# Optimization experiments

Hardware: AMD Instinct MI355X
Metric: run time of the kernel (lower is better)

The kernel has to match this reference:

```python
import jax, jax.numpy as jnp
import numpy as np

PS = 8        # window/patch size (win_size)
STRIDE = 4    # overlapping-window stride
HEADS = 2


def _rel_pos_index(ps):
    ch = np.arange(ps)
    coords = np.stack(np.meshgrid(ch, ch, indexing='ij'))  # (2, ps, ps)
    cf = coords.reshape(2, -1)
    rel = cf[:, :, None] - cf[:, None, :]                   # (2, L, L)
    rel = rel.transpose(1, 2, 0).copy()
    rel[:, :, 0] += ps - 1
    rel[:, :, 1] += ps - 1
    rel[:, :, 0] *= 2 * ps - 1
    return rel.sum(-1).astype(np.int32)                     # (L, L)


def setup_inputs() -> dict:
    key = jax.random.key(0)
    ks = jax.random.split(key, 6)
    t, h, w, c = 8, 128, 128, 32
    inp = {
        'x': jax.random.normal(ks[0], (t, h, w, c), jnp.float32),
        'qkv_w': jax.random.normal(ks[1], (3 * c, c), jnp.float32) * (c ** -0.5),
        'qkv_b': jnp.zeros((3 * c,), jnp.float32),
        'rel_pos_table': jax.random.normal(ks[2], ((2 * PS - 1) ** 2, HEADS), jnp.float32) * 0.02,
        'proj_w': jax.random.normal(ks[3], (c, c), jnp.float32) * (c ** -0.5),
        'proj_b': jnp.zeros((c,), jnp.float32),
        'rel_pos_index': jnp.asarray(_rel_pos_index(PS)),
    }
    return inp


def reference(x, qkv_w, qkv_b, rel_pos_table, proj_w, proj_b, rel_pos_index):
    t, h, w, c = x.shape
    hd = c // HEADS
    scale = hd ** -0.5
    L = PS * PS
    nh = (h - 1) // STRIDE + 1
    nw = (w - 1) // STRIDE + 1

    # --- iUnfold: gather overlapping ps x ps patches with reflected borders ---
    r0 = jnp.arange(nh) * STRIDE
    c0 = jnp.arange(nw) * STRIDE
    ridx = r0[:, None] + jnp.arange(PS)[None, :]            # (nh, ps)
    cidx = c0[:, None] + jnp.arange(PS)[None, :]            # (nw, ps)
    ridx = jnp.where(ridx >= h, 2 * (h - 1) - ridx, ridx)
    cidx = jnp.where(cidx >= w, 2 * (w - 1) - cidx, cidx)
    # advanced indexing -> (t, nh, nw, ps, ps, c)
    patches = x[:, ridx[:, None, :, None], cidx[None, :, None, :], :]
    n = t * nh * nw
    patches = patches.reshape(n, L, c)

    # --- LinearProjection qkv ---
    qkv = patches @ qkv_w.T + qkv_b                          # (n, L, 3c)
    q, k, v = jnp.split(qkv, 3, axis=-1)
    def heads(a):
        return a.reshape(n, L, HEADS, hd).transpose(0, 2, 1, 3)  # (n, H, L, hd)
    q, k, v = heads(q), heads(k), heads(v)

    # --- scaled attention + indexed relative position bias ---
    attn = jnp.einsum('nhld,nhmd->nhlm', q * scale, k)       # (n, H, L, L)
    bias = rel_pos_table[rel_pos_index]                      # (L, L, H)
    attn = jax.nn.softmax(attn + bias.transpose(2, 0, 1)[None], axis=-1)
    out = jnp.einsum('nhlm,nhmd->nhld', attn, v)             # (n, H, L, hd)
    out = out.transpose(0, 2, 1, 3).reshape(n, L, c)
    out = out @ proj_w.T + proj_b

    # --- iFold: scatter-add with overlap-count (wfold) normalization ---
    lin = (ridx[:, None, :, None] * w + cidx[None, :, None, :]).reshape(-1)  # (nh*nw*L,)
    vals = out.reshape(t, nh * nw * L, c)
    vid = jnp.zeros((t, h * w, c), x.dtype).at[:, lin, :].add(vals)
    cnt = jnp.zeros((h * w,), x.dtype).at[lin].add(1.0)
    vid = vid / (cnt[None, :, None] + 1e-10)
    return vid.reshape(t, h, w, c)
```

## Files before the change

### kernel.cpp

```cpp
#include <hip/hip_runtime.h>
#include <hip/hip_bf16.h>
#include <stdint.h>

typedef __attribute__((ext_vector_type(8))) short bf16x8;
typedef __attribute__((ext_vector_type(4))) float f32x4;

#define LOG2E 1.44269504088896340736f
#define QSCALE (0.25f * LOG2E)

#define WS_BIASF 0u
#define WS_QKVW  32768u
#define WS_PROJW 38912u
#define WS_QKVB  40960u
#define WS_OUT   41472u
#define NEED_FULL (41472ull + 8192ull*64*32*2)

#define PWAVE 4096

__device__ __forceinline__ uint32_t pk2(float a, float b){
    union{__hip_bfloat162 h;uint32_t u;}c;
    c.h=__float22bfloat162_rn(make_float2(a,b)); return c.u;
}
template<int OFF>
__device__ __forceinline__ uint2 tr16(uint32_t a){
    uint2 d;
    asm volatile("ds_read_b64_tr_b16 %0, %1 offset:%2" : "=v"(d) : "v"(a), "i"(OFF) : "memory");
    return d;
}
__device__ __forceinline__ void lgkm0(){
    asm volatile("s_waitcnt lgkmcnt(0)" ::: "memory");
    __builtin_amdgcn_sched_barrier(0);
}
__device__ __forceinline__ bf16x8 mk8u(uint2 a, uint2 b){
    union{bf16x8 v;uint32_t u[4];}z; z.u[0]=a.x; z.u[1]=a.y; z.u[2]=b.x; z.u[3]=b.y; return z.v;
}
__device__ __forceinline__ bf16x8 mk8q(uint32_t q0, uint32_t q1, uint32_t q2, uint32_t q3){
    union{bf16x8 v;uint32_t u[4];}z; z.u[0]=q0; z.u[1]=q1; z.u[2]=q2; z.u[3]=q3; return z.v;
}
__device__ __forceinline__ void pl32(uint32_t &a, uint32_t &b){
    asm volatile("v_permlane32_swap_b32 %0, %1" : "+v"(a), "+v"(b));
}
__device__ __forceinline__ void pl16(uint32_t &a, uint32_t &b){
    asm volatile("v_permlane16_swap_b32 %0, %1" : "+v"(a), "+v"(b));
}
__device__ __forceinline__ f32x4 mfma16(uint2 a, uint2 b, f32x4 c){
    asm("v_mfma_f32_16x16x16_bf16 %0, %1, %2, %0" : "+v"(c) : "v"(a), "v"(b));
    return c;
}

__global__ __launch_bounds__(256) void prep(const float* __restrict__ qkv_w,
                                            const float* __restrict__ qkv_b,
                                            const float* __restrict__ rel_tab,
                                            const float* __restrict__ proj_w,
                                            char* __restrict__ ws)
{
    int t = blockIdx.x*256 + threadIdx.x;
    if (t < 2048) {
        int lanei = t & 63, tile = t >> 6;
        int h = tile >> 4, nt = (tile >> 2) & 3, mt = tile & 3;
        int gg = lanei >> 4, lnn = lanei & 15;
        int l = 16*nt + lnn;
        f32x4 v;
        #pragma unroll
        for (int r = 0; r < 4; ++r) {
            int m = 16*mt + 4*gg + r;
            int dr = (l >> 3) - (m >> 3) + 7;
            int dc = (l & 7) - (m & 7) + 7;
            v[r] = rel_tab[(dr*15 + dc)*2 + h] * LOG2E;
        }
        *(f32x4*)(ws + WS_BIASF + (size_t)t*16) = v;
    } else if (t < 3584) {
        int e = (t - 2048) * 2;
        int row = e >> 5;
        float s = (row < 32) ? QSCALE : 1.0f;
        *(uint32_t*)(ws + WS_QKVW + e*2) = pk2(qkv_w[e]*s, qkv_w[e+1]*s);
    } else {
        int e = (t - 3584) * 2;
        *(uint32_t*)(ws + WS_PROJW + e*2) = pk2(proj_w[e], proj_w[e+1]);
    }
    if (t < 96) {
        float s = (t < 32) ? QSCALE : 1.0f;
        ((float*)(ws + WS_QKVB))[t] = qkv_b[t] * s;
    }
}

template<int WSPATH>
__global__ __launch_bounds__(128, 4) void win_attn(
    const float* __restrict__ x, const float* __restrict__ proj_b,
    const char* __restrict__ wsc, uint16_t* __restrict__ wout,
    float* __restrict__ out)
{
    __shared__ __align__(16) char smem_all[2*PWAVE];
    const int tid = threadIdx.x;
    const int wv = tid >> 6, lane = tid & 63;
    const int g = lane >> 4, ln = lane & 15;
    const int bid = blockIdx.x;
    const int sb = (bid & 7) * 512 + (bid >> 3);
    const int wid = sb * 2 + wv;
    const int t_i = wid >> 10, wi = (wid >> 5) & 31, wj = wid & 31;
    char* smem = smem_all + wv * PWAVE;
    const uint32_t Lb = (uint32_t)(uintptr_t)(&smem[0]);

    const f32x4* biasF = (const f32x4*)(wsc + WS_BIASF);
    const uint16_t* wbf = (const uint16_t*)(wsc + WS_QKVW);
    const float* qbs = (const float*)(wsc + WS_QKVB);

    int pixb[4];
    #pragma unroll
    for (int i = 0; i < 4; ++i) {
        int tok = 16*i + ln, pr = tok >> 3, pc = tok & 7;
        int ar = wi*4 + pr; if (ar >= 128) ar = 254 - ar;
        int ac = wj*4 + pc; if (ac >= 128) ac = 254 - ac;
        pixb[i] = (t_i*128 + ar)*128 + ac;
    }

    bf16x8 xf[4];
    #pragma unroll
    for (int nt = 0; nt < 4; ++nt) {
        const float4* p = (const float4*)(x + (size_t)pixb[nt]*32 + 8*g);
        float4 a = p[0], b = p[1];
        union{bf16x8 v; uint32_t u[4];} z;
        z.u[0]=pk2(a.x,a.y); z.u[1]=pk2(a.z,a.w);
        z.u[2]=pk2(b.x,b.y); z.u[3]=pk2(b.z,b.w);
        xf[nt] = z.v;
    }

    uint2 qk[4][4];
    #pragma unroll
    for (int mt = 0; mt < 6; ++mt) {
        bf16x8 wf = *(const bf16x8*)(wbf + (ln + 16*mt)*32 + 8*g);
        float4 qb = *(const float4*)(qbs + 16*mt + 4*g);
        #pragma unroll
        for (int nt = 0; nt < 4; ++nt) {
            f32x4 acc = {qb.x, qb.y, qb.z, qb.w};
            acc = __builtin_amdgcn_mfma_f32_16x16x32_bf16(wf, xf[nt], acc, 0, 0, 0);
            if (mt < 4) {
                qk[mt][nt].x = pk2(acc[0], acc[1]);
                qk[mt][nt].y = pk2(acc[2], acc[3]);
            } else {
                int tok = 16*nt + ln;
                uint2 u; u.x = pk2(acc[0], acc[1]); u.y = pk2(acc[2], acc[3]);
                *(uint2*)(smem + (mt-4)*2048 + tok*32 + 8*g) = u;
            }
        }
    }

    const uint32_t one2 = 0x3f803f80u;
    const bf16x8 ones = mk8q(one2, one2, one2, one2);

    #pragma unroll
    for (int h = 0; h < 2; ++h) {
        uint32_t va = Lb + h*2048 + 256*g + 8*ln;
        uint2 v00 = tr16<0>(va),    v01 = tr16<128>(va);
        uint2 v10 = tr16<1024>(va), v11 = tr16<1152>(va);
        lgkm0();
        bf16x8 vb0 = mk8u(v00, v01), vb1 = mk8u(v10, v11);

        f32x4 bpc[4];
        #pragma unroll
        for (int mt = 0; mt < 4; ++mt)
            bpc[mt] = biasF[((h*4 + 0)*4 + mt)*64 + lane];

        #pragma unroll
        for (int nt = 0; nt < 4; ++nt) {
            f32x4 bpn[4];
            const int ntn = (nt < 3) ? nt + 1 : 3;
            #pragma unroll
            for (int mt = 0; mt < 4; ++mt)
                bpn[mt] = biasF[((h*4 + ntn)*4 + mt)*64 + lane];

            __builtin_amdgcn_s_setprio(1);
            f32x4 sc[4];
            #pragma unroll
            for (int mt = 0; mt < 4; ++mt)
                sc[mt] = mfma16(qk[2+h][mt], qk[h][nt], bpc[mt]);
            __builtin_amdgcn_s_setprio(0);

            #pragma unroll
            for (int mt = 0; mt < 4; ++mt) {
                sc[mt][0]=__builtin_amdgcn_exp2f(sc[mt][0]);
                sc[mt][1]=__builtin_amdgcn_exp2f(sc[mt][1]);
                sc[mt][2]=__builtin_amdgcn_exp2f(sc[mt][2]);
                sc[mt][3]=__builtin_amdgcn_exp2f(sc[mt][3]);
            }

            uint32_t pkA[4], pkB[4];
            #pragma unroll
            for (int mt = 0; mt < 4; ++mt) {
                pkA[mt] = pk2(sc[mt][0], sc[mt][1]);
                pkB[mt] = pk2(sc[mt][2], sc[mt][3]);
            }
            uint32_t a0 = pkA[0], a1 = pkA[1]; pl32(a0, a1); pl16(a0, a1);
            uint32_t b0 = pkB[0], b1 = pkB[1]; pl32(b0, b1); pl16(b0, b1);
            bf16x8 pa0 = mk8q(a0, b0, a1, b1);
            uint32_t a2 = pkA[2], a3 = pkA[3]; pl32(a2, a3); pl16(a2, a3);
            uint32_t b2 = pkB[2], b3 = pkB[3]; pl32(b2, b3); pl16(b2, b3);
            bf16x8 pa1 = mk8q(a2, b2, a3, b3);

            __builtin_amdgcn_s_setprio(1);
            f32x4 z = {0.f,0.f,0.f,0.f};
            z = __builtin_amdgcn_mfma_f32_16x16x32_bf16(pa0, vb0, z, 0, 0, 0);
            f32x4 oc = __builtin_amdgcn_mfma_f32_16x16x32_bf16(pa1, vb1, z, 0, 0, 0);
            f32x4 sm = {0.f,0.f,0.f,0.f};
            sm = __builtin_amdgcn_mfma_f32_16x16x32_bf16(pa0, ones, sm, 0, 0, 0);
            sm = __builtin_amdgcn_mfma_f32_16x16x32_bf16(pa1, ones, sm, 0, 0, 0);
            __builtin_amdgcn_s_setprio(0);

            oc[0] *= __builtin_amdgcn_rcpf(sm[0]);
            oc[1] *= __builtin_amdgcn_rcpf(sm[1]);
            oc[2] *= __builtin_amdgcn_rcpf(sm[2]);
            oc[3] *= __builtin_amdgcn_rcpf(sm[3]);

            uint2 u; u.x = pk2(oc[0], oc[1]); u.y = pk2(oc[2], oc[3]);
            *(uint2*)(smem + h*2048 + (nt*4 + (ln>>2))*128 + (ln&3)*32 + 8*g) = u;

            #pragma unroll
            for (int mt = 0; mt < 4; ++mt) bpc[mt] = bpn[mt];
        }
    }

    const uint16_t* pwbf = (const uint16_t*)(wsc + WS_PROJW);
    bf16x8 w2f[2];
    w2f[0] = *(const bf16x8*)(pwbf + ln*32 + 8*g);
    w2f[1] = *(const bf16x8*)(pwbf + (16 + ln)*32 + 8*g);
    float4 pbv[2];
    pbv[0] = *(const float4*)(proj_b + 4*g);
    pbv[1] = *(const float4*)(proj_b + 16 + 4*g);

    uint32_t ob = Lb + ((uint32_t)(g >> 1) << 11) + ((uint32_t)(g & 1) << 8) + 8*ln;
    uint2 a0=tr16<0>(ob),    a1=tr16<128>(ob);
    uint2 b0=tr16<512>(ob),  b1=tr16<640>(ob);
    uint2 c0=tr16<1024>(ob), c1=tr16<1152>(ob);
    uint2 d0=tr16<1536>(ob), d1=tr16<1664>(ob);
    lgkm0();
    bf16x8 oa[4];
    oa[0]=mk8u(a0,a1); oa[1]=mk8u(b0,b1); oa[2]=mk8u(c0,c1); oa[3]=mk8u(d0,d1);

    #pragma unroll
    for (int mt2 = 0; mt2 < 2; ++mt2) {
        #pragma unroll
        for (int nt = 0; nt < 4; ++nt) {
            f32x4 acc = {pbv[mt2].x, pbv[mt2].y, pbv[mt2].z, pbv[mt2].w};
            acc = __builtin_amdgcn_mfma_f32_16x16x32_bf16(w2f[mt2], oa[nt], acc, 0, 0, 0);
            if (WSPATH) {
                uint2 u; u.x = pk2(acc[0], acc[1]); u.y = pk2(acc[2], acc[3]);
                *(uint2*)(wout + ((size_t)wid*64 + 16*nt + ln)*32 + 16*mt2 + 4*g) = u;
            } else {
                #pragma unroll
                for (int r = 0; r < 4; ++r)
                    atomicAdd(out + (size_t)pixb[nt]*32 + 16*mt2 + 4*g + r, acc[r]);
            }
        }
    }
}

__global__ __launch_bounds__(256) void gather_out(const uint16_t* __restrict__ ws,
                                                  float* __restrict__ out)
{
    int gid = blockIdx.x * 256 + threadIdx.x;
    int q = gid & 7;
    int c = (gid >> 3) & 127;
    int r = (gid >> 10) & 127;
    int t = gid >> 17;

    int wr[3], pr[3], nr = 0;
    { int w0 = r >> 2;
      wr[0] = w0; pr[0] = r & 3; nr = 1;
      if (w0 >= 1) { wr[nr] = w0 - 1; pr[nr] = (r & 3) + 4; nr++; }
      if (r >= 123 && r <= 126) { wr[nr] = 31; pr[nr] = 130 - r; nr++; } }
    int wc[3], pc[3], nc = 0;
    { int w0 = c >> 2;
      wc[0] = w0; pc[0] = c & 3; nc = 1;
      if (w0 >= 1) { wc[nc] = w0 - 1; pc[nc] = (c & 3) + 4; nc++; }
      if (c >= 123 && c <= 126) { wc[nc] = 31; pc[nc] = 130 - c; nc++; } }

    float4 acc; acc.x = acc.y = acc.z = acc.w = 0.f;
    #pragma unroll
    for (int i = 0; i < 3; ++i) {
        #pragma unroll
        for (int j = 0; j < 3; ++j) {
            if (i < nr && j < nc) {
                int win = t*1024 + wr[i]*32 + wc[j];
                int tok = pr[i]*8 + pc[j];
                ushort4 v = *reinterpret_cast<const ushort4*>(ws + ((size_t)win*64 + tok)*32 + q*4);
                union { uint32_t u; float f; } a0,a1,a2,a3;
                a0.u = (uint32_t)v.x << 16; a1.u = (uint32_t)v.y << 16;
                a2.u = (uint32_t)v.z << 16; a3.u = (uint32_t)v.w << 16;
                acc.x += a0.f; acc.y += a1.f; acc.z += a2.f; acc.w += a3.f;
            }
        }
    }
    float inv = __builtin_amdgcn_rcpf((float)(nr*nc));
    acc.x *= inv; acc.y *= inv; acc.z *= inv; acc.w *= inv;
    reinterpret_cast<float4*>(out)[gid] = acc;
}

__global__ __launch_bounds__(256) void div_kernel(float* __restrict__ out)
{
    int gid = blockIdx.x*blockDim.x + threadIdx.x;
    const int total4 = 8*128*128*32/4;
    if (gid >= total4) return;
    int pix = gid >> 3;
    int c_ = pix % 128;
    int r_ = (pix / 128) % 128;
    int cr = 0, cc = 0;
    for (int i = 0; i < 32; ++i) {
        #pragma unroll
        for (int p = 0; p < 8; ++p) {
            int rr = i*4 + p; if (rr >= 128) rr = 254 - rr;
            cr += (rr == r_);
            int aa = i*4 + p; if (aa >= 128) aa = 254 - aa;
            cc += (aa == c_);
        }
    }
    float inv = 1.f / ((float)cr*(float)cc + 1e-10f);
    float4* p4 = reinterpret_cast<float4*>(out) + gid;
    float4 v = *p4;
    v.x *= inv; v.y *= inv; v.z *= inv; v.w *= inv;
    *p4 = v;
}

extern "C" void kernel_launch(void* const* d_in, const int* in_sizes, int n_in,
                              void* d_out, int out_size, void* d_ws, size_t ws_size,
                              hipStream_t stream) {
    const float* x       = (const float*)d_in[0];
    const float* qkv_w   = (const float*)d_in[1];
    const float* qkv_b   = (const float*)d_in[2];
    const float* rel_tab = (const float*)d_in[3];
    const float* proj_w  = (const float*)d_in[4];
    const float* proj_b  = (const float*)d_in[5];
    float* out = (float*)d_out;
    char* ws = (char*)d_ws;

    prep<<<16, 256, 0, stream>>>(qkv_w, qkv_b, rel_tab, proj_w, ws);

    if (ws_size >= NEED_FULL) {
        win_attn<1><<<4096, 128, 0, stream>>>(x, proj_b, (const char*)ws,
                                              (uint16_t*)(ws + WS_OUT), out);
        gather_out<<<4096, 256, 0, stream>>>((const uint16_t*)(ws + WS_OUT), out);
    } else {
        hipMemsetAsync(out, 0, (size_t)out_size*sizeof(float), stream);
        win_attn<0><<<4096, 128, 0, stream>>>(x, proj_b, (const char*)ws, nullptr, out);
        const int tot4 = 8*128*128*32/4;
        div_kernel<<<(tot4 + 255)/256, 256, 0, stream>>>(out);
    }
}
```

Before: 50.31 us.

## Split attention heads across waves, one wave per head per window

The window-attention kernel now runs 256 threads per block, with two waves per window, each handling one attention head. Each wave computes only its head's Q, K and V projection, runs that head's attention, then after a block barrier computes half of the output projection channels. The intent is more wave-level parallelism and a shorter serial chain per wave, with fewer live registers per wave. The cost is that each pair of waves loads the same input pixels twice, plus a __syncthreads before the projection.

```diff
diff --git a/kernel.cpp b/kernel.cpp
--- a/kernel.cpp
+++ b/kernel.cpp
@@ -15,7 +15,7 @@
 #define WS_OUT   41472u
 #define NEED_FULL (41472ull + 8192ull*64*32*2)
 
-#define PWAVE 4096
+#define PWIN 4096
 
 __device__ __forceinline__ uint32_t pk2(float a, float b){
     union{__hip_bfloat162 h;uint32_t u;}c;
@@ -85,20 +85,21 @@
 }
 
 template<int WSPATH>
-__global__ __launch_bounds__(128, 4) void win_attn(
+__global__ __launch_bounds__(256, 6) void win_attn(
     const float* __restrict__ x, const float* __restrict__ proj_b,
     const char* __restrict__ wsc, uint16_t* __restrict__ wout,
     float* __restrict__ out)
 {
-    __shared__ __align__(16) char smem_all[2*PWAVE];
+    __shared__ __align__(16) char smem_all[2*PWIN];
     const int tid = threadIdx.x;
-    const int wv = tid >> 6, lane = tid & 63;
+    const int w = tid >> 6, lane = tid & 63;
+    const int wvwin = w & 1, h = w >> 1;
     const int g = lane >> 4, ln = lane & 15;
     const int bid = blockIdx.x;
     const int sb = (bid & 7) * 512 + (bid >> 3);
-    const int wid = sb * 2 + wv;
+    const int wid = sb * 2 + wvwin;
     const int t_i = wid >> 10, wi = (wid >> 5) & 31, wj = wid & 31;
-    char* smem = smem_all + wv * PWAVE;
+    char* smem = smem_all + wvwin * PWIN;
     const uint32_t Lb = (uint32_t)(uintptr_t)(&smem[0]);
 
     const f32x4* biasF = (const f32x4*)(wsc + WS_BIASF);
@@ -125,22 +126,26 @@
         xf[nt] = z.v;
     }
 
-    uint2 qk[4][4];
-    #pragma unroll
-    for (int mt = 0; mt < 6; ++mt) {
-        bf16x8 wf = *(const bf16x8*)(wbf + (ln + 16*mt)*32 + 8*g);
-        float4 qb = *(const float4*)(qbs + 16*mt + 4*g);
+    uint2 qkQ[4], qkK[4];
+    #pragma unroll
+    for (int j = 0; j < 3; ++j) {
+        const int mtw = 2*j + h;
+        bf16x8 wf = *(const bf16x8*)(wbf + (ln + 16*mtw)*32 + 8*g);
+        float4 qb = *(const float4*)(qbs + 16*mtw + 4*g);
         #pragma unroll
         for (int nt = 0; nt < 4; ++nt) {
             f32x4 acc = {qb.x, qb.y, qb.z, qb.w};
             acc = __builtin_amdgcn_mfma_f32_16x16x32_bf16(wf, xf[nt], acc, 0, 0, 0);
-            if (mt < 4) {
-                qk[mt][nt].x = pk2(acc[0], acc[1]);
-                qk[mt][nt].y = pk2(acc[2], acc[3]);
+            if (j == 0) {
+                qkQ[nt].x = pk2(acc[0], acc[1]);
+                qkQ[nt].y = pk2(acc[2], acc[3]);
+            } else if (j == 1) {
+                qkK[nt].x = pk2(acc[0], acc[1]);
+                qkK[nt].y = pk2(acc[2], acc[3]);
             } else {
                 int tok = 16*nt + ln;
                 uint2 u; u.x = pk2(acc[0], acc[1]); u.y = pk2(acc[2], acc[3]);
-                *(uint2*)(smem + (mt-4)*2048 + tok*32 + 8*g) = u;
+                *(uint2*)(smem + h*2048 + tok*32 + 8*g) = u;
             }
         }
     }
@@ -148,84 +153,79 @@
     const uint32_t one2 = 0x3f803f80u;
     const bf16x8 ones = mk8q(one2, one2, one2, one2);
 
-    #pragma unroll
-    for (int h = 0; h < 2; ++h) {
-        uint32_t va = Lb + h*2048 + 256*g + 8*ln;
-        uint2 v00 = tr16<0>(va),    v01 = tr16<128>(va);
-        uint2 v10 = tr16<1024>(va), v11 = tr16<1152>(va);
-        lgkm0();
-        bf16x8 vb0 = mk8u(v00, v01), vb1 = mk8u(v10, v11);
-
-        f32x4 bpc[4];
+    uint32_t va = Lb + h*2048 + 256*g + 8*ln;
+    uint2 v00 = tr16<0>(va),    v01 = tr16<128>(va);
+    uint2 v10 = tr16<1024>(va), v11 = tr16<1152>(va);
+    lgkm0();
+    bf16x8 vb0 = mk8u(v00, v01), vb1 = mk8u(v10, v11);
+
+    f32x4 bpc[4];
+    #pragma unroll
+    for (int mt = 0; mt < 4; ++mt)
+        bpc[mt] = biasF[((h*4 + 0)*4 + mt)*64 + lane];
+
+    #pragma unroll
+    for (int nt = 0; nt < 4; ++nt) {
+        f32x4 bpn[4];
+        const int ntn = (nt < 3) ? nt + 1 : 3;
         #pragma unroll
         for (int mt = 0; mt < 4; ++mt)
-            bpc[mt] = biasF[((h*4 + 0)*4 + mt)*64 + lane];
-
-        #pragma unroll
-        for (int nt = 0; nt < 4; ++nt) {
-            f32x4 bpn[4];
-            const int ntn = (nt < 3) ? nt + 1 : 3;
-            #pragma unroll
-            for (int mt = 0; mt < 4; ++mt)
-                bpn[mt] = biasF[((h*4 + ntn)*4 + mt)*64 + lane];
-
-            __builtin_amdgcn_s_setprio(1);
-            f32x4 sc[4];
-            #pragma unroll
-            for (int mt = 0; mt < 4; ++mt)
-                sc[mt] = mfma16(qk[2+h][mt], qk[h][nt], bpc[mt]);
-            __builtin_amdgcn_s_setprio(0);
-
-            #pragma unroll
-            for (int mt = 0; mt < 4; ++mt) {
-                sc[mt][0]=__builtin_amdgcn_exp2f(sc[mt][0]);
-                sc[mt][1]=__builtin_amdgcn_exp2f(sc[mt][1]);
-                sc[mt][2]=__builtin_amdgcn_exp2f(sc[mt][2]);
-                sc[mt][3]=__builtin_amdgcn_exp2f(sc[mt][3]);
-            }
-
-            uint32_t pkA[4], pkB[4];
-            #pragma unroll
-            for (int mt = 0; mt < 4; ++mt) {
-                pkA[mt] = pk2(sc[mt][0], sc[mt][1]);
-                pkB[mt] = pk2(sc[mt][2], sc[mt][3]);
-            }
-            uint32_t a0 = pkA[0], a1 = pkA[1]; pl32(a0, a1); pl16(a0, a1);
-            uint32_t b0 = pkB[0], b1 = pkB[1]; pl32(b0, b1); pl16(b0, b1);
-            bf16x8 pa0 = mk8q(a0, b0, a1, b1);
-            uint32_t a2 = pkA[2], a3 = pkA[3]; pl32(a2, a3); pl16(a2, a3);
-            uint32_t b2 = pkB[2], b3 = pkB[3]; pl32(b2, b3); pl16(b2, b3);
-            bf16x8 pa1 = mk8q(a2, b2, a3, b3);
-
-            __builtin_amdgcn_s_setprio(1);
-            f32x4 z = {0.f,0.f,0.f,0.f};
-            z = __builtin_amdgcn_mfma_f32_16x16x32_bf16(pa0, vb0, z, 0, 0, 0);
-            f32x4 oc = __builtin_amdgcn_mfma_f32_16x16x32_bf16(pa1, vb1, z, 0, 0, 0);
-            f32x4 sm = {0.f,0.f,0.f,0.f};
-            sm = __builtin_amdgcn_mfma_f32_16x16x32_bf16(pa0, ones, sm, 0, 0, 0);
-            sm = __builtin_amdgcn_mfma_f32_16x16x32_bf16(pa1, ones, sm, 0, 0, 0);
-            __builtin_amdgcn_s_setprio(0);
-
-            oc[0] *= __builtin_amdgcn_rcpf(sm[0]);
-            oc[1] *= __builtin_amdgcn_rcpf(sm[1]);
-            oc[2] *= __builtin_amdgcn_rcpf(sm[2]);
-            oc[3] *= __builtin_amdgcn_rcpf(sm[3]);
-
-            uint2 u; u.x = pk2(oc[0], oc[1]); u.y = pk2(oc[2], oc[3]);
-            *(uint2*)(smem + h*2048 + (nt*4 + (ln>>2))*128 + (ln&3)*32 + 8*g) = u;
-
-            #pragma unroll
-            for (int mt = 0; mt < 4; ++mt) bpc[mt] = bpn[mt];
-        }
-    }
+            bpn[mt] = biasF[((h*4 + ntn)*4 + mt)*64 + lane];
+
+        __builtin_amdgcn_s_setprio(1);
+        f32x4 sc[4];
+        #pragma unroll
+        for (int mt = 0; mt < 4; ++mt)
+            sc[mt] = mfma16(qkK[mt], qkQ[nt], bpc[mt]);
+        __builtin_amdgcn_s_setprio(0);
+
+        #pragma unroll
+        for (int mt = 0; mt < 4; ++mt) {
+            sc[mt][0]=__builtin_amdgcn_exp2f(sc[mt][0]);
+            sc[mt][1]=__builtin_amdgcn_exp2f(sc[mt][1]);
+            sc[mt][2]=__builtin_amdgcn_exp2f(sc[mt][2]);
+            sc[mt][3]=__builtin_amdgcn_exp2f(sc[mt][3]);
+        }
+
+        uint32_t pkA[4], pkB[4];
+        #pragma unroll
+        for (int mt = 0; mt < 4; ++mt) {
+            pkA[mt] = pk2(sc[mt][0], sc[mt][1]);
+            pkB[mt] = pk2(sc[mt][2], sc[mt][3]);
+        }
+        uint32_t a0 = pkA[0], a1 = pkA[1]; pl32(a0, a1); pl16(a0, a1);
+        uint32_t b0 = pkB[0], b1 = pkB[1]; pl32(b0, b1); pl16(b0, b1);
+        bf16x8 pa0 = mk8q(a0, b0, a1, b1);
+        uint32_t a2 = pkA[2], a3 = pkA[3]; pl32(a2, a3); pl16(a2, a3);
+        uint32_t b2 = pkB[2], b3 = pkB[3]; pl32(b2, b3); pl16(b2, b3);
+        bf16x8 pa1 = mk8q(a2, b2, a3, b3);
+
+        __builtin_amdgcn_s_setprio(1);
+        f32x4 z = {0.f,0.f,0.f,0.f};
+        z = __builtin_amdgcn_mfma_f32_16x16x32_bf16(pa0, vb0, z, 0, 0, 0);
+        f32x4 oc = __builtin_amdgcn_mfma_f32_16x16x32_bf16(pa1, vb1, z, 0, 0, 0);
+        f32x4 sm = {0.f,0.f,0.f,0.f};
+        sm = __builtin_amdgcn_mfma_f32_16x16x32_bf16(pa0, ones, sm, 0, 0, 0);
+        sm = __builtin_amdgcn_mfma_f32_16x16x32_bf16(pa1, ones, sm, 0, 0, 0);
+        __builtin_amdgcn_s_setprio(0);
+
+        oc[0] *= __builtin_amdgcn_rcpf(sm[0]);
+        oc[1] *= __builtin_amdgcn_rcpf(sm[1]);
+        oc[2] *= __builtin_amdgcn_rcpf(sm[2]);
+        oc[3] *= __builtin_amdgcn_rcpf(sm[3]);
+
+        uint2 u; u.x = pk2(oc[0], oc[1]); u.y = pk2(oc[2], oc[3]);
+        *(uint2*)(smem + h*2048 + (nt*4 + (ln>>2))*128 + (ln&3)*32 + 8*g) = u;
+
+        #pragma unroll
+        for (int mt = 0; mt < 4; ++mt) bpc[mt] = bpn[mt];
+    }
+
+    __syncthreads();
 
     const uint16_t* pwbf = (const uint16_t*)(wsc + WS_PROJW);
-    bf16x8 w2f[2];
-    w2f[0] = *(const bf16x8*)(pwbf + ln*32 + 8*g);
-    w2f[1] = *(const bf16x8*)(pwbf + (16 + ln)*32 + 8*g);
-    float4 pbv[2];
-    pbv[0] = *(const float4*)(proj_b + 4*g);
-    pbv[1] = *(const float4*)(proj_b + 16 + 4*g);
+    bf16x8 w2f = *(const bf16x8*)(pwbf + (16*h + ln)*32 + 8*g);
+    float4 pbv = *(const float4*)(proj_b + 16*h + 4*g);
 
     uint32_t ob = Lb + ((uint32_t)(g >> 1) << 11) + ((uint32_t)(g & 1) << 8) + 8*ln;
     uint2 a0=tr16<0>(ob),    a1=tr16<128>(ob);
@@ -237,19 +237,16 @@
     oa[0]=mk8u(a0,a1); oa[1]=mk8u(b0,b1); oa[2]=mk8u(c0,c1); oa[3]=mk8u(d0,d1);
 
     #pragma unroll
-    for (int mt2 = 0; mt2 < 2; ++mt2) {
-        #pragma unroll
-        for (int nt = 0; nt < 4; ++nt) {
-            f32x4 acc = {pbv[mt2].x, pbv[mt2].y, pbv[mt2].z, pbv[mt2].w};
-            acc = __builtin_amdgcn_mfma_f32_16x16x32_bf16(w2f[mt2], oa[nt], acc, 0, 0, 0);
-            if (WSPATH) {
-                uint2 u; u.x = pk2(acc[0], acc[1]); u.y = pk2(acc[2], acc[3]);
-                *(uint2*)(wout + ((size_t)wid*64 + 16*nt + ln)*32 + 16*mt2 + 4*g) = u;
-            } else {
-                #pragma unroll
-                for (int r = 0; r < 4; ++r)
-                    atomicAdd(out + (size_t)pixb[nt]*32 + 16*mt2 + 4*g + r, acc[r]);
-            }
+    for (int nt = 0; nt < 4; ++nt) {
+        f32x4 acc = {pbv.x, pbv.y, pbv.z, pbv.w};
+        acc = __builtin_amdgcn_mfma_f32_16x16x32_bf16(w2f, oa[nt], acc, 0, 0, 0);
+        if (WSPATH) {
+            uint2 u; u.x = pk2(acc[0], acc[1]); u.y = pk2(acc[2], acc[3]);
+            *(uint2*)(wout + ((size_t)wid*64 + 16*nt + ln)*32 + 16*h + 4*g) = u;
+        } else {
+            #pragma unroll
+            for (int r = 0; r < 4; ++r)
+                atomicAdd(out + (size_t)pixb[nt]*32 + 16*h + 4*g + r, acc[r]);
         }
     }
 }
@@ -335,12 +332,12 @@
     prep<<<16, 256, 0, stream>>>(qkv_w, qkv_b, rel_tab, proj_w, ws);
 
     if (ws_size >= NEED_FULL) {
-        win_attn<1><<<4096, 128, 0, stream>>>(x, proj_b, (const char*)ws,
+        win_attn<1><<<4096, 256, 0, stream>>>(x, proj_b, (const char*)ws,
                                               (uint16_t*)(ws + WS_OUT), out);
         gather_out<<<4096, 256, 0, stream>>>((const uint16_t*)(ws + WS_OUT), out);
     } else {
         hipMemsetAsync(out, 0, (size_t)out_size*sizeof(float), stream);
-        win_attn<0><<<4096, 128, 0, stream>>>(x, proj_b, (const char*)ws, nullptr, out);
+        win_attn<0><<<4096, 256, 0, stream>>>(x, proj_b, (const char*)ws, nullptr, out);
         const int tot4 = 8*128*128*32/4;
         div_kernel<<<(tot4 + 255)/256, 256, 0, stream>>>(out);
     }
```

Result: slower. 55.67 us (+10.6%).

## Defer output projection past fold averaging and preload all bias tiles

Applied to the files above, without the earlier changes.

The output projection is linear, so it is moved out of the attention kernel and applied once per pixel after the overlapping-window averaging. The attention kernel now stores pre-projection activations, and a new finish kernel gathers, averages and projects them via MFMA. This aims to cut the projection MFMA count, since each pixel was projected several times before, and to trim per-window work. Bias tiles are preloaded all at once per head and the launch-bounds occupancy hint is lowered to 3, which raises register use in exchange for fewer dependent loads. The finish kernel launches 512 blocks, far fewer than before, so that step may be latency-bound.

```diff
diff --git a/kernel.cpp b/kernel.cpp
--- a/kernel.cpp
+++ b/kernel.cpp
@@ -85,7 +85,7 @@
 }
 
 template<int WSPATH>
-__global__ __launch_bounds__(128, 4) void win_attn(
+__global__ __launch_bounds__(128, 3) void win_attn(
     const float* __restrict__ x, const float* __restrict__ proj_b,
     const char* __restrict__ wsc, uint16_t* __restrict__ wout,
     float* __restrict__ out)
@@ -150,30 +150,24 @@
 
     #pragma unroll
     for (int h = 0; h < 2; ++h) {
+        f32x4 bp[16];
+        #pragma unroll
+        for (int t2 = 0; t2 < 16; ++t2)
+            bp[t2] = biasF[(h*16 + t2)*64 + lane];
+
         uint32_t va = Lb + h*2048 + 256*g + 8*ln;
         uint2 v00 = tr16<0>(va),    v01 = tr16<128>(va);
         uint2 v10 = tr16<1024>(va), v11 = tr16<1152>(va);
         lgkm0();
         bf16x8 vb0 = mk8u(v00, v01), vb1 = mk8u(v10, v11);
 
-        f32x4 bpc[4];
-        #pragma unroll
-        for (int mt = 0; mt < 4; ++mt)
-            bpc[mt] = biasF[((h*4 + 0)*4 + mt)*64 + lane];
-
         #pragma unroll
         for (int nt = 0; nt < 4; ++nt) {
-            f32x4 bpn[4];
-            const int ntn = (nt < 3) ? nt + 1 : 3;
-            #pragma unroll
-            for (int mt = 0; mt < 4; ++mt)
-                bpn[mt] = biasF[((h*4 + ntn)*4 + mt)*64 + lane];
-
             __builtin_amdgcn_s_setprio(1);
             f32x4 sc[4];
             #pragma unroll
             for (int mt = 0; mt < 4; ++mt)
-                sc[mt] = mfma16(qk[2+h][mt], qk[h][nt], bpc[mt]);
+                sc[mt] = mfma16(qk[2+h][mt], qk[h][nt], bp[nt*4 + mt]);
             __builtin_amdgcn_s_setprio(0);
 
             #pragma unroll
@@ -213,19 +207,8 @@
 
             uint2 u; u.x = pk2(oc[0], oc[1]); u.y = pk2(oc[2], oc[3]);
             *(uint2*)(smem + h*2048 + (nt*4 + (ln>>2))*128 + (ln&3)*32 + 8*g) = u;
-
-            #pragma unroll
-            for (int mt = 0; mt < 4; ++mt) bpc[mt] = bpn[mt];
-        }
-    }
-
-    const uint16_t* pwbf = (const uint16_t*)(wsc + WS_PROJW);
-    bf16x8 w2f[2];
-    w2f[0] = *(const bf16x8*)(pwbf + ln*32 + 8*g);
-    w2f[1] = *(const bf16x8*)(pwbf + (16 + ln)*32 + 8*g);
-    float4 pbv[2];
-    pbv[0] = *(const float4*)(proj_b + 4*g);
-    pbv[1] = *(const float4*)(proj_b + 16 + 4*g);
+        }
+    }
 
     uint32_t ob = Lb + ((uint32_t)(g >> 1) << 11) + ((uint32_t)(g & 1) << 8) + 8*ln;
     uint2 a0=tr16<0>(ob),    a1=tr16<128>(ob);
@@ -236,63 +219,111 @@
     bf16x8 oa[4];
     oa[0]=mk8u(a0,a1); oa[1]=mk8u(b0,b1); oa[2]=mk8u(c0,c1); oa[3]=mk8u(d0,d1);
 
+    if (WSPATH) {
+        #pragma unroll
+        for (int nt = 0; nt < 4; ++nt)
+            *(bf16x8*)(wout + ((size_t)wid*64 + 16*nt + ln)*32 + 8*g) = oa[nt];
+    } else {
+        const uint16_t* pwbf = (const uint16_t*)(wsc + WS_PROJW);
+        bf16x8 w2f[2];
+        w2f[0] = *(const bf16x8*)(pwbf + ln*32 + 8*g);
+        w2f[1] = *(const bf16x8*)(pwbf + (16 + ln)*32 + 8*g);
+        float4 pbv[2];
+        pbv[0] = *(const float4*)(proj_b + 4*g);
+        pbv[1] = *(const float4*)(proj_b + 16 + 4*g);
+        #pragma unroll
+        for (int mt2 = 0; mt2 < 2; ++mt2) {
+            #pragma unroll
+            for (int nt = 0; nt < 4; ++nt) {
+                f32x4 acc = {pbv[mt2].x, pbv[mt2].y, pbv[mt2].z, pbv[mt2].w};
+                acc = __builtin_amdgcn_mfma_f32_16x16x32_bf16(w2f[mt2], oa[nt], acc, 0, 0, 0);
+                #pragma unroll
+                for (int r = 0; r < 4; ++r)
+                    atomicAdd(out + (size_t)pixb[nt]*32 + 16*mt2 + 4*g + r, acc[r]);
+            }
+        }
+    }
+}
+
+__global__ __launch_bounds__(256) void finish_kernel(const uint16_t* __restrict__ ws,
+                                                     const char* __restrict__ wsc,
+                                                     const float* __restrict__ proj_b,
+                                                     float* __restrict__ out)
+{
+    __shared__ __align__(16) char smem[20480];
+    const int tid = threadIdx.x;
+    const int wv = tid >> 6, lane = tid & 63;
+    const int g = lane >> 4, ln = lane & 15;
+    const int pix0 = (blockIdx.x * 4 + wv) * 64;
+    const int p = pix0 + lane;
+    const int c = p & 127, r = (p >> 7) & 127, t_i = p >> 14;
+    char* Ls = smem + wv * 5120;
+
+    float s[32];
+    #pragma unroll
+    for (int q = 0; q < 32; ++q) s[q] = 0.f;
+
+    int wr[3], pr[3], nr = 0;
+    { int w0 = r >> 2;
+      wr[0]=w0; pr[0]=r&3; nr=1;
+      if (w0 >= 1) { wr[nr]=w0-1; pr[nr]=(r&3)+4; nr++; }
+      if (r >= 123 && r <= 126) { wr[nr]=31; pr[nr]=130-r; nr++; } }
+    int wc[3], pc[3], nc = 0;
+    { int w0 = c >> 2;
+      wc[0]=w0; pc[0]=c&3; nc=1;
+      if (w0 >= 1) { wc[nc]=w0-1; pc[nc]=(c&3)+4; nc++; }
+      if (c >= 123 && c <= 126) { wc[nc]=31; pc[nc]=130-c; nc++; } }
+
+    #pragma unroll
+    for (int i = 0; i < 3; ++i) {
+        #pragma unroll
+        for (int j = 0; j < 3; ++j) {
+            if (i < nr && j < nc) {
+                int win = t_i*1024 + wr[i]*32 + wc[j];
+                int tok = pr[i]*8 + pc[j];
+                const uint32_t* ab = (const uint32_t*)(ws + ((size_t)win*64 + tok)*32);
+                #pragma unroll
+                for (int q = 0; q < 16; ++q) {
+                    uint32_t u = ab[q];
+                    union{uint32_t uu; float f;} lo, hi;
+                    lo.uu = u << 16; hi.uu = u & 0xffff0000u;
+                    s[2*q]   += lo.f;
+                    s[2*q+1] += hi.f;
+                }
+            }
+        }
+    }
+    float inv = __builtin_amdgcn_rcpf((float)(nr*nc));
+    #pragma unroll
+    for (int q = 0; q < 4; ++q) {
+        uint4 u;
+        u.x = pk2(s[8*q+0]*inv, s[8*q+1]*inv);
+        u.y = pk2(s[8*q+2]*inv, s[8*q+3]*inv);
+        u.z = pk2(s[8*q+4]*inv, s[8*q+5]*inv);
+        u.w = pk2(s[8*q+6]*inv, s[8*q+7]*inv);
+        *(uint4*)(Ls + lane*80 + 16*q) = u;
+    }
+    __syncthreads();
+    const uint16_t* pwbf = (const uint16_t*)(wsc + WS_PROJW);
+    bf16x8 w2f[2];
+    w2f[0] = *(const bf16x8*)(pwbf + ln*32 + 8*g);
+    w2f[1] = *(const bf16x8*)(pwbf + (16 + ln)*32 + 8*g);
+    float4 pbv[2];
+    pbv[0] = *(const float4*)(proj_b + 4*g);
+    pbv[1] = *(const float4*)(proj_b + 16 + 4*g);
+    bf16x8 oa[4];
+    #pragma unroll
+    for (int nt = 0; nt < 4; ++nt)
+        oa[nt] = *(const bf16x8*)(Ls + (ln + 16*nt)*80 + 16*g);
     #pragma unroll
     for (int mt2 = 0; mt2 < 2; ++mt2) {
         #pragma unroll
         for (int nt = 0; nt < 4; ++nt) {
             f32x4 acc = {pbv[mt2].x, pbv[mt2].y, pbv[mt2].z, pbv[mt2].w};
             acc = __builtin_amdgcn_mfma_f32_16x16x32_bf16(w2f[mt2], oa[nt], acc, 0, 0, 0);
-            if (WSPATH) {
-                uint2 u; u.x = pk2(acc[0], acc[1]); u.y = pk2(acc[2], acc[3]);
-                *(uint2*)(wout + ((size_t)wid*64 + 16*nt + ln)*32 + 16*mt2 + 4*g) = u;
-            } else {
-                #pragma unroll
-                for (int r = 0; r < 4; ++r)
-                    atomicAdd(out + (size_t)pixb[nt]*32 + 16*mt2 + 4*g + r, acc[r]);
-            }
-        }
-    }
-}
-
-__global__ __launch_bounds__(256) void gather_out(const uint16_t* __restrict__ ws,
-                                                  float* __restrict__ out)
-{
-    int gid = blockIdx.x * 256 + threadIdx.x;
-    int q = gid & 7;
-    int c = (gid >> 3) & 127;
-    int r = (gid >> 10) & 127;
-    int t = gid >> 17;
-
-    int wr[3], pr[3], nr = 0;
-    { int w0 = r >> 2;
-      wr[0] = w0; pr[0] = r & 3; nr = 1;
-      if (w0 >= 1) { wr[nr] = w0 - 1; pr[nr] = (r & 3) + 4; nr++; }
-      if (r >= 123 && r <= 126) { wr[nr] = 31; pr[nr] = 130 - r; nr++; } }
-    int wc[3], pc[3], nc = 0;
-    { int w0 = c >> 2;
-      wc[0] = w0; pc[0] = c & 3; nc = 1;
-      if (w0 >= 1) { wc[nc] = w0 - 1; pc[nc] = (c & 3) + 4; nc++; }
-      if (c >= 123 && c <= 126) { wc[nc] = 31; pc[nc] = 130 - c; nc++; } }
-
-    float4 acc; acc.x = acc.y = acc.z = acc.w = 0.f;
-    #pragma unroll
-    for (int i = 0; i < 3; ++i) {
-        #pragma unroll
-        for (int j = 0; j < 3; ++j) {
-            if (i < nr && j < nc) {
-                int win = t*1024 + wr[i]*32 + wc[j];
-                int tok = pr[i]*8 + pc[j];
-                ushort4 v = *reinterpret_cast<const ushort4*>(ws + ((size_t)win*64 + tok)*32 + q*4);
-                union { uint32_t u; float f; } a0,a1,a2,a3;
-                a0.u = (uint32_t)v.x << 16; a1.u = (uint32_t)v.y << 16;
-                a2.u = (uint32_t)v.z << 16; a3.u = (uint32_t)v.w << 16;
-                acc.x += a0.f; acc.y += a1.f; acc.z += a2.f; acc.w += a3.f;
-            }
-        }
-    }
-    float inv = __builtin_amdgcn_rcpf((float)(nr*nc));
-    acc.x *= inv; acc.y *= inv; acc.z *= inv; acc.w *= inv;
-    reinterpret_cast<float4*>(out)[gid] = acc;
+            *(f32x4*)(out + (size_t)(pix0 + 16*nt + ln)*32 + 16*mt2 + 4*g) = acc;
+        }
+    }
 }
 
 __global__ __launch_bounds__(256) void div_kernel(float* __restrict__ out)
@@ -337,7 +368,8 @@
     if (ws_size >= NEED_FULL) {
         win_attn<1><<<4096, 128, 0, stream>>>(x, proj_b, (const char*)ws,
                                               (uint16_t*)(ws + WS_OUT), out);
-        gather_out<<<4096, 256, 0, stream>>>((const uint16_t*)(ws + WS_OUT), out);
+        finish_kernel<<<512, 256, 0, stream>>>((const uint16_t*)(ws + WS_OUT),
+                                               (const char*)ws, proj_b, out);
     } else {
         hipMemsetAsync(out, 0, (size_t)out_size*sizeof(float), stream);
         win_attn<0><<<4096, 128, 0, stream>>>(x, proj_b, (const char*)ws, nullptr, out);
```

New measurement: 51.20 us. About the same (+1.8%).
